# Optimization experiments

Hardware: AMD Instinct MI355X
Metric: run time of the kernel (lower is better)

## Reference

```python
import jax, jax.numpy as jnp
import numpy as np

T = 2048          # tokens (flattened prefill)
H = 3584          # hidden_size
NH = 16           # num query heads
NKV = 8           # num kv heads
G = NH // NKV     # GQA group size
D = 256           # head_dim
SCALE = 256.0 ** -0.5   # query_pre_attn_scalar ** -0.5
WINDOW = 1024     # sliding_window_size
CAP = 50.0        # logit softcap
BASE = 10000.0    # rope theta
NEG = -1e30


def _rope(x, positions):
    # x: [T, n, D], neox-style rotary over full head_dim
    half = D // 2
    inv_freq = 1.0 / (BASE ** (jnp.arange(0, D, 2, dtype=jnp.float32) / D))  # [half]
    ang = positions.astype(jnp.float32)[:, None] * inv_freq  # [T, half]
    cos = jnp.cos(ang)[:, None, :]  # [T,1,half]
    sin = jnp.sin(ang)[:, None, :]
    x1, x2 = x[..., :half], x[..., half:]
    return jnp.concatenate([x1 * cos - x2 * sin, x2 * cos + x1 * sin], axis=-1)


def setup_inputs() -> dict:
    key = jax.random.key(0)
    ks = jax.random.split(key, 5)
    s = 0.02
    return {
        "hidden_states": jax.random.normal(ks[0], (T, H), dtype=jnp.float32),
        "Wq": jax.random.normal(ks[1], (H, NH * D), dtype=jnp.float32) * s,
        "Wk": jax.random.normal(ks[2], (H, NKV * D), dtype=jnp.float32) * s,
        "Wv": jax.random.normal(ks[3], (H, NKV * D), dtype=jnp.float32) * s,
        "Wo": jax.random.normal(ks[4], (NH * D, H), dtype=jnp.float32) * s,
        "positions": jnp.arange(T, dtype=jnp.int32),
    }


def reference(hidden_states, Wq, Wk, Wv, Wo, positions):
    q = (hidden_states @ Wq).reshape(T, NH, D)
    k = (hidden_states @ Wk).reshape(T, NKV, D)
    v = (hidden_states @ Wv).reshape(T, NKV, D)
    q = _rope(q, positions)
    k = _rope(k, positions)

    # GQA attention: group query heads over kv heads
    qg = (q * SCALE).reshape(T, NKV, G, D)
    scores = jnp.einsum('qhgd,khd->hgqk', qg, k)  # [NKV,G,T,T]
    scores = CAP * jnp.tanh(scores / CAP)         # logit softcap

    i = jnp.arange(T)[:, None]
    j = jnp.arange(T)[None, :]
    mask = (j <= i) & (i - j < WINDOW)            # causal + sliding window
    scores = jnp.where(mask, scores, NEG)

    p = jax.nn.softmax(scores, axis=-1)
    o = jnp.einsum('hgqk,khd->qhgd', p, v).reshape(T, NH * D)
    return o @ Wo
```

## Files before the change

### kernel.cpp

```cpp
#include <hip/hip_runtime.h>
#include <math.h>

typedef __attribute__((ext_vector_type(8))) __bf16 bf16x8;
typedef __attribute__((ext_vector_type(4))) __bf16 bf16x4;
typedef __attribute__((ext_vector_type(4))) float f32x4;

#define TSEQ 2048
#define HDIM 3584
#define NQH  16
#define NKVH 8
#define DH   256
#define WIN  1024
#define QKD  (NQH * DH)
#define KVD  (NKVH * DH)
#define QLD  8256
#define OLD  4160
#define WOLD 4160
#define VLD  2112

#define MFMA __builtin_amdgcn_mfma_f32_16x16x32_bf16

__device__ __forceinline__ void gload_lds16(const void* g, void* l) {
  __builtin_amdgcn_global_load_lds(
      (const __attribute__((address_space(1))) void*)g,
      (__attribute__((address_space(3))) void*)l, 16, 0, 0);
}


__global__ void cvt_bf16_kernel(const float* __restrict__ in,
                                __bf16* __restrict__ out, long n) {
  long i = ((long)blockIdx.x * blockDim.x + threadIdx.x) * 4;
  if (i >= n) return;
  float4 v = *reinterpret_cast<const float4*>(in + i);
  bf16x4 o4;
  o4.x = (__bf16)v.x; o4.y = (__bf16)v.y; o4.z = (__bf16)v.z; o4.w = (__bf16)v.w;
  *reinterpret_cast<bf16x4*>(out + i) = o4;
}

__global__ void transpose_all_kernel(const float* __restrict__ Wq,
                                     const float* __restrict__ Wk,
                                     const float* __restrict__ Wv,
                                     const float* __restrict__ Wo,
                                     __bf16* __restrict__ WqT,
                                     __bf16* __restrict__ WkT,
                                     __bf16* __restrict__ WvT,
                                     __bf16* __restrict__ WoT) {
  __shared__ float tile[64][65];
  int id = blockIdx.x;
  const float* src; __bf16* dst; int R, C, ldo;
  if (id < 3584)      { src = Wq; dst = WqT; R = HDIM; C = QKD; ldo = HDIM; }
  else if (id < 5376) { id -= 3584; src = Wk; dst = WkT; R = HDIM; C = KVD; ldo = HDIM; }
  else if (id < 7168) { id -= 5376; src = Wv; dst = WvT; R = HDIM; C = KVD; ldo = HDIM; }
  else                { id -= 7168; src = Wo; dst = WoT; R = QKD; C = HDIM; ldo = WOLD; }
  const int nbx = C >> 6;
  const int c0 = (id % nbx) * 64, r0 = (id / nbx) * 64;
  const int tid = threadIdx.x;
#pragma unroll
  for (int it = 0; it < 4; ++it) {
    int f = tid + it * 256;
    int row = f >> 4, c4 = (f & 15) * 4;
    float4 v = *reinterpret_cast<const float4*>(&src[(size_t)(r0 + row) * C + c0 + c4]);
    tile[row][c4] = v.x; tile[row][c4 + 1] = v.y;
    tile[row][c4 + 2] = v.z; tile[row][c4 + 3] = v.w;
  }
  __syncthreads();
#pragma unroll
  for (int it = 0; it < 2; ++it) {
    int s = tid + it * 256;
    int oc = s >> 3, rb = (s & 7) * 8;
    bf16x8 o8;
#pragma unroll
    for (int j = 0; j < 8; ++j) o8[j] = (__bf16)tile[rb + j][oc];
    *reinterpret_cast<bf16x8*>(&dst[(size_t)(c0 + oc) * ldo + r0 + rb]) = o8;
  }
}

__global__ void transpose_bf16_kernel(const __bf16* __restrict__ in,
                                      __bf16* __restrict__ out, int ldin, int ldout) {
  __shared__ __bf16 tile[32][33];
  const int tx = threadIdx.x, ty = threadIdx.y;
  const int c0 = blockIdx.x * 32, r0 = blockIdx.y * 32;
#pragma unroll
  for (int i = 0; i < 4; ++i)
    tile[ty + i * 8][tx] = in[(size_t)(r0 + ty + i * 8) * ldin + (c0 + tx)];
  __syncthreads();
#pragma unroll
  for (int i = 0; i < 4; ++i)
    out[(size_t)(c0 + ty + i * 8) * ldout + (r0 + tx)] = tile[tx][ty + i * 8];
}

__global__ void rope_table_kernel(const int* __restrict__ positions,
                                  float* __restrict__ ct,
                                  float* __restrict__ st) {
  int i = blockIdx.x * blockDim.x + threadIdx.x;
  if (i >= TSEQ * 128) return;
  int t = i >> 7, j = i & 127;
  float invf = (float)exp((double)(-2 * j) * (9.210340371976184 / 256.0));
  float ang = (float)positions[t] * invf;
  ct[i] = cosf(ang);
  st[i] = sinf(ang);
}

__global__ void rope_qk_kernel(__bf16* __restrict__ qkv,
                               const float* __restrict__ ct,
                               const float* __restrict__ st) {
  int i = blockIdx.x * blockDim.x + threadIdx.x;
  int jg = (i & 15) * 8;
  int th = i >> 4;
  int t = th / 24;
  int hh = th - t * 24;
  float scale = (hh < 16) ? 0.0625f : 1.0f;
  size_t base = (size_t)t * QLD + ((hh < 16) ? hh * DH : QKD + (hh - 16) * DH) + jg;
  bf16x8 x1 = *reinterpret_cast<const bf16x8*>(qkv + base);
  bf16x8 x2 = *reinterpret_cast<const bf16x8*>(qkv + base + 128);
  const float* cp = ct + (t << 7) + jg;
  const float* sp = st + (t << 7) + jg;
  bf16x8 o1, o2;
#pragma unroll
  for (int e = 0; e < 8; ++e) {
    float c = cp[e], s = sp[e];
    float a = (float)x1[e], b = (float)x2[e];
    o1[e] = (__bf16)((a * c - b * s) * scale);
    o2[e] = (__bf16)((b * c + a * s) * scale);
  }
  *reinterpret_cast<bf16x8*>(qkv + base) = o1;
  *reinterpret_cast<bf16x8*>(qkv + base + 128) = o2;
}

__global__ void reduce2_kernel(const __bf16* __restrict__ p0,
                               const __bf16* __restrict__ p1,
                               float* __restrict__ out, int n8) {
  int stride = gridDim.x * blockDim.x;
  for (int i = blockIdx.x * blockDim.x + threadIdx.x; i < n8; i += stride) {
    bf16x8 a = reinterpret_cast<const bf16x8*>(p0)[i];
    bf16x8 b = reinterpret_cast<const bf16x8*>(p1)[i];
    float4 o0, o1;
    o0.x = (float)a[0] + (float)b[0]; o0.y = (float)a[1] + (float)b[1];
    o0.z = (float)a[2] + (float)b[2]; o0.w = (float)a[3] + (float)b[3];
    o1.x = (float)a[4] + (float)b[4]; o1.y = (float)a[5] + (float)b[5];
    o1.z = (float)a[6] + (float)b[6]; o1.w = (float)a[7] + (float)b[7];
    reinterpret_cast<float4*>(out)[2 * i] = o0;
    reinterpret_cast<float4*>(out)[2 * i + 1] = o1;
  }
}


__device__ __forceinline__ void stage_half(const __bf16* __restrict__ gbase,
                                           int row0, int ldg, int k0,
                                           __bf16* lds_half, int tid) {
  const int lane = tid & 63;
  const int w = tid >> 6;
  const int lr = lane >> 3;
  const int swzcol = ((lane & 7) ^ lr) << 3;
  const __bf16* g = gbase + (size_t)(row0 + w * 8 + lr) * ldg + k0 + swzcol;
  __bf16* l = lds_half + w * 512;
  gload_lds16(g, l);
  gload_lds16(g + (size_t)64 * ldg, l + 4096);
}

#define BAR __builtin_amdgcn_s_barrier()

#define RD_A(DST, BASE, MO)                                         \
  _Pragma("unroll")                                                 \
  for (int m_ = 0; m_ < 4; ++m_) {                                  \
    const __bf16* p_ = (BASE) + (((MO) + m_) * 16 + l15) * 64;      \
    DST[m_][0] = *(const bf16x8*)(p_ + kxa);                        \
    DST[m_][1] = *(const bf16x8*)(p_ + kxb);                        \
  }

#define RD_B(DST, BASE, NO)                                         \
  _Pragma("unroll")                                                 \
  for (int n_ = 0; n_ < 2; ++n_) {                                  \
    const __bf16* p_ = (BASE) + (bro + ((NO) + n_) * 16 + l15) * 64;\
    DST[n_][0] = *(const bf16x8*)(p_ + kxa);                        \
    DST[n_][1] = *(const bf16x8*)(p_ + kxb);                        \
  }

#define MQUAD(AF, BF, MO, NO)                                          \
  __builtin_amdgcn_s_setprio(1);                                       \
  _Pragma("unroll")                                                    \
  for (int m_ = 0; m_ < 4; ++m_)                                       \
    _Pragma("unroll")                                                  \
    for (int n_ = 0; n_ < 2; ++n_) {                                   \
      acc[(MO) + m_][(NO) + n_] =                                      \
          MFMA(AF[m_][0], BF[n_][0], acc[(MO) + m_][(NO) + n_], 0, 0, 0); \
      acc[(MO) + m_][(NO) + n_] =                                      \
          MFMA(AF[m_][1], BF[n_][1], acc[(MO) + m_][(NO) + n_], 0, 0, 0); \
    }                                                                  \
  __builtin_amdgcn_s_setprio(0);

template <typename CT>
__global__ __launch_bounds__(512, 2) void gemm256_kernel(
    const __bf16* __restrict__ A, const __bf16* __restrict__ B,
    CT* __restrict__ C, int lda, int Klen, int ldc, int nrc, size_t cstride) {
  __shared__ __bf16 lds[2][2][2][8192];

  const int nwg = gridDim.x;
  const int per = nwg >> 3;
  const int wg = (blockIdx.x & 7) * per + (blockIdx.x >> 3);
  const int kslice = wg / nrc;
  const int rem = wg - kslice * nrc;
  const int row0 = (rem & 7) * 256;
  const int col0 = (rem >> 3) * 256;
  const int k0 = kslice * Klen;
  CT* Cs = C + (size_t)kslice * cstride;

  const int tid = threadIdx.x;
  const int lane = tid & 63, w = tid >> 6;
  const int wr = w >> 2, wc = w & 3;
  const int l15 = lane & 15, lg = lane >> 4;
  const int swz = (lane & 7) << 3;
  const int kxa = (lg * 8) ^ swz;
  const int kxb = (32 + lg * 8) ^ swz;
  const int bro = (wc & 1) * 64;

  const __bf16* Ablk = A + (size_t)row0 * lda + k0;
  const __bf16* Bblk = B + (size_t)col0 * lda + k0;

  const __bf16* Ae = &lds[0][0][wr][0];
  const __bf16* Be = &lds[0][1][wc >> 1][0];
  const __bf16* Ao = &lds[1][0][wr][0];
  const __bf16* Bo = &lds[1][1][wc >> 1][0];

  f32x4 acc[8][4] = {};
  const int NT = Klen >> 6;
  const int NI = NT >> 1;

  stage_half(Ablk, 0,   lda, 0,  &lds[0][0][0][0], tid);
  stage_half(Ablk, 128, lda, 0,  &lds[0][0][1][0], tid);
  stage_half(Bblk, 0,   lda, 0,  &lds[0][1][0][0], tid);
  stage_half(Bblk, 128, lda, 0,  &lds[0][1][1][0], tid);
  stage_half(Ablk, 0,   lda, 64, &lds[1][0][0][0], tid);
  stage_half(Ablk, 128, lda, 64, &lds[1][0][1][0], tid);
  asm volatile("s_waitcnt vmcnt(4)" ::: "memory");
  BAR;

  bf16x8 a03[4][2], a47[4][2], b01[2][2], b23[2][2];

  for (int j = 0; j < NI; ++j) {
    const int e = 2 * j, o = 2 * j + 1;
    const bool last = (j == NI - 1);

    RD_A(a03, Ae, 0);
    RD_B(b01, Be, 0);
    stage_half(Bblk, 0, lda, o * 64, &lds[1][1][0][0], tid);
    asm volatile("s_waitcnt lgkmcnt(8)" ::: "memory");
    BAR; MQUAD(a03, b01, 0, 0); BAR;

    RD_A(a47, Ae, 4);
    stage_half(Bblk, 128, lda, o * 64, &lds[1][1][1][0], tid);
    BAR; MQUAD(a47, b01, 4, 0); BAR;

    RD_B(b23, Be, 2);
    if (!last) stage_half(Ablk, 0, lda, (e + 2) * 64, &lds[0][0][0][0], tid);
    BAR; MQUAD(a47, b23, 4, 2); BAR;

    if (!last) {
      stage_half(Ablk, 128, lda, (e + 2) * 64, &lds[0][0][1][0], tid);
      asm volatile("s_waitcnt vmcnt(4)" ::: "memory");
    } else {
      asm volatile("s_waitcnt vmcnt(0)" ::: "memory");
    }
    BAR; MQUAD(a03, b23, 0, 2); BAR;

    RD_A(a03, Ao, 0);
    RD_B(b01, Bo, 0);
    if (!last) stage_half(Bblk, 0, lda, (e + 2) * 64, &lds[0][1][0][0], tid);
    asm volatile("s_waitcnt lgkmcnt(8)" ::: "memory");
    BAR; MQUAD(a03, b01, 0, 0); BAR;

    RD_A(a47, Ao, 4);
    if (!last) stage_half(Bblk, 128, lda, (e + 2) * 64, &lds[0][1][1][0], tid);
    BAR; MQUAD(a47, b01, 4, 0); BAR;

    RD_B(b23, Bo, 2);
    if (!last) stage_half(Ablk, 0, lda, (o + 2) * 64, &lds[1][0][0][0], tid);
    BAR; MQUAD(a47, b23, 4, 2); BAR;

    if (!last) {
      stage_half(Ablk, 128, lda, (o + 2) * 64, &lds[1][0][1][0], tid);
      asm volatile("s_waitcnt vmcnt(4)" ::: "memory");
    }
    BAR; MQUAD(a03, b23, 0, 2); BAR;
  }

#pragma unroll
  for (int m = 0; m < 8; ++m)
#pragma unroll
    for (int n = 0; n < 4; ++n)
#pragma unroll
      for (int r = 0; r < 4; ++r) {
        int row = row0 + wr * 128 + m * 16 + lg * 4 + r;
        int col = col0 + wc * 64 + n * 16 + l15;
        Cs[(size_t)row * ldc + col] = (CT)acc[m][n][r];
      }
}


__device__ __forceinline__ void attn_stage(const __bf16* __restrict__ kg,
                                           const __bf16* __restrict__ vg,
                                           __bf16* Kd, __bf16* Vd, int tid) {
#pragma unroll
  for (int i = 0; i < 8; ++i) {
    int c = tid + i * 256;
    int krow = c >> 5, kslot = c & 31;
    gload_lds16(kg + (size_t)krow * QLD + ((kslot ^ (krow & 7)) * 8), Kd + c * 8);
    int vrow = c >> 3, vslot = c & 7;
    gload_lds16(vg + (size_t)vrow * VLD + ((vslot ^ (vrow & 7)) * 8), Vd + c * 8);
  }
}

__global__ __launch_bounds__(256, 2) void attn_kernel(
    const __bf16* __restrict__ q, const __bf16* __restrict__ k,
    const __bf16* __restrict__ vt, __bf16* __restrict__ o) {
  __shared__ __bf16 Klds[64][256];
  __shared__ __bf16 Vlds[256][64];
  __shared__ __bf16 Plds[4][16][72];

  const int tid = threadIdx.x;
  const int wave = tid >> 6;
  const int lane = tid & 63;
  const int l16 = lane & 15;
  const int lg = lane >> 4;
  const int h = blockIdx.x;
  const int qh = 2 * h + (blockIdx.y & 1);
  const int q0 = (31 - (int)(blockIdx.y >> 1)) << 6;
  const int qr = q0 + wave * 16;

  const __bf16* kg0 = k + (size_t)h * DH;
  const __bf16* vg0 = vt + (size_t)(h * DH) * VLD;

  int t_lo = q0 - (WIN - 1);
  if (t_lo < 0) t_lo = 0;
  t_lo &= ~63;
  const int NTile = ((q0 - t_lo) >> 6) + 1;

  bf16x8 qf[8];
  {
    const __bf16* qp = q + (size_t)(qr + l16) * QLD + qh * DH + lg * 8;
#pragma unroll
    for (int ds = 0; ds < 8; ++ds)
      qf[ds] = *reinterpret_cast<const bf16x8*>(qp + ds * 32);
  }

  f32x4 accO[16] = {};
  float l_run[4] = {0.f, 0.f, 0.f, 0.f};

  for (int it = 0; it < NTile; ++it) {
    const int t0 = t_lo + it * 64;

    attn_stage(kg0 + (size_t)t0 * QLD, vg0 + t0, &Klds[0][0], &Vlds[0][0], tid);
    asm volatile("s_waitcnt vmcnt(0)" ::: "memory");
    __builtin_amdgcn_s_barrier();

    f32x4 accS[4] = {};
    __builtin_amdgcn_s_setprio(1);
#pragma unroll
    for (int ds = 0; ds < 8; ++ds)
#pragma unroll
      for (int nt = 0; nt < 4; ++nt) {
        int row = nt * 16 + l16;
        int slot = (4 * ds + lg) ^ (l16 & 7);
        bf16x8 kf = *reinterpret_cast<const bf16x8*>(&Klds[0][0] + row * 256 + slot * 8);
        accS[nt] = MFMA(qf[ds], kf, accS[nt], 0, 0, 0);
      }
    __builtin_amdgcn_s_setprio(0);

    float rs[4] = {0.f, 0.f, 0.f, 0.f};
#pragma unroll
    for (int nt = 0; nt < 4; ++nt) {
      int key = t0 + nt * 16 + l16;
#pragma unroll
      for (int r = 0; r < 4; ++r) {
        int row = qr + lg * 4 + r;
        float t = __expf(accS[nt][r] * 0.04f);
        float p = __expf(-100.0f / (t + 1.0f));
        bool valid = (key <= row) && (row - key < WIN);
        p = valid ? p : 0.f;
        rs[r] += p;
        Plds[wave][lg * 4 + r][nt * 16 + l16] = (__bf16)p;
      }
    }
#pragma unroll
    for (int off = 1; off < 16; off <<= 1)
#pragma unroll
      for (int r = 0; r < 4; ++r)
        rs[r] += __shfl_xor(rs[r], off);
#pragma unroll
    for (int r = 0; r < 4; ++r)
      l_run[r] += rs[r];

    __builtin_amdgcn_s_setprio(1);
#pragma unroll
    for (int ks = 0; ks < 2; ++ks) {
      bf16x8 pa = *reinterpret_cast<const bf16x8*>(&Plds[wave][l16][ks * 32 + lg * 8]);
#pragma unroll
      for (int nt2 = 0; nt2 < 16; ++nt2) {
        int row = nt2 * 16 + l16;
        int slot = (4 * ks + lg) ^ (l16 & 7);
        bf16x8 vb = *reinterpret_cast<const bf16x8*>(&Vlds[0][0] + row * 64 + slot * 8);
        accO[nt2] = MFMA(pa, vb, accO[nt2], 0, 0, 0);
      }
    }
    __builtin_amdgcn_s_setprio(0);
    __builtin_amdgcn_s_barrier();
  }

#pragma unroll
  for (int r = 0; r < 4; ++r) {
    float inv_l = 1.f / l_run[r];
    int row = qr + lg * 4 + r;
#pragma unroll
    for (int nt2 = 0; nt2 < 16; ++nt2)
      o[(size_t)row * OLD + qh * DH + nt2 * 16 + l16] = (__bf16)(accO[nt2][r] * inv_l);
  }
}


extern "C" void kernel_launch(void* const* d_in, const int* in_sizes, int n_in,
                              void* d_out, int out_size, void* d_ws, size_t ws_size,
                              hipStream_t stream) {
  const float* hs = (const float*)d_in[0];
  const float* Wq = (const float*)d_in[1];
  const float* Wk = (const float*)d_in[2];
  const float* Wv = (const float*)d_in[3];
  const float* Wo = (const float*)d_in[4];
  const int* positions = (const int*)d_in[5];
  float* out = (float*)d_out;

  char* ws = (char*)d_ws;
  const size_t SZ_HS  = (size_t)TSEQ * HDIM * 2;
  const size_t SZ_WQT = (size_t)QKD * HDIM * 2;
  const size_t SZ_WKT = (size_t)KVD * HDIM * 2;
  const size_t SZ_WOT = (size_t)HDIM * WOLD * 2;
  const size_t SZ_QKV = (size_t)TSEQ * QLD * 2;
  const size_t SZ_O   = (size_t)TSEQ * OLD * 2;
  const size_t SZ_TBL = (size_t)TSEQ * 128 * 4;

  __bf16* hs_bf = (__bf16*)ws; ws += SZ_HS;
  __bf16* WqT   = (__bf16*)ws; ws += SZ_WQT;
  __bf16* WkT   = (__bf16*)ws; ws += SZ_WKT;
  __bf16* WvT   = (__bf16*)ws; ws += SZ_WKT;
  __bf16* WoT   = (__bf16*)ws; ws += SZ_WOT;
  __bf16* qkv   = (__bf16*)ws; ws += SZ_QKV;
  __bf16* o_bf  = (__bf16*)ws; ws += SZ_O;
  float*  cost  = (float*)ws;  ws += SZ_TBL;
  float*  sint  = (float*)ws;  ws += SZ_TBL;
  __bf16* vt_bf = hs_bf;
  __bf16* cpart = WqT;
  if ((size_t)(ws - (char*)d_ws) > ws_size) return;

  cvt_bf16_kernel<<<(TSEQ * HDIM) / 1024, 256, 0, stream>>>(hs, hs_bf, (long)TSEQ * HDIM);
  transpose_all_kernel<<<10752, 256, 0, stream>>>(Wq, Wk, Wv, Wo, WqT, WkT, WvT, WoT);
  rope_table_kernel<<<(TSEQ * 128) / 256, 256, 0, stream>>>(positions, cost, sint);

  gemm256_kernel<__bf16><<<256, 512, 0, stream>>>(hs_bf, WqT, qkv, HDIM, HDIM, QLD, 256, 0);

  rope_qk_kernel<<<(TSEQ * 24 * 16) / 256, 256, 0, stream>>>(qkv, cost, sint);
  transpose_bf16_kernel<<<dim3(KVD / 32, TSEQ / 32), dim3(32, 8), 0, stream>>>(qkv + QKD + KVD, vt_bf, QLD, VLD);

  attn_kernel<<<dim3(NKVH, 64), 256, 0, stream>>>(qkv, qkv + QKD, vt_bf, o_bf);

  gemm256_kernel<__bf16><<<224, 512, 0, stream>>>(o_bf, WoT, cpart, OLD, QKD / 2, HDIM, 112,
                                                  (size_t)TSEQ * HDIM);
  reduce2_kernel<<<2048, 256, 0, stream>>>(cpart, cpart + (size_t)TSEQ * HDIM, out,
                                           TSEQ * HDIM / 8);
}
```

Before: 304.4 us.

## Replace split-K output projection with 128x256-tile GEMM writing fp32 directly

The output projection previously ran as a split-K GEMM with 256x256 tiles into two bf16 partial buffers, followed by a separate reduction kernel. It now uses a new 128x256-tile GEMM over the full K that writes fp32 output directly, which removes the partial-buffer traffic, the reduce launch and one bf16 rounding. The new kernel uses a different LDS double-buffer pipeline and allows one workgroup per CU. Each workgroup now runs twice as many K iterations on a smaller tile, which lowers MFMA work per LDS load.

```diff
diff --git a/kernel.cpp b/kernel.cpp
--- a/kernel.cpp
+++ b/kernel.cpp
@@ -127,23 +127,6 @@
   *reinterpret_cast<bf16x8*>(qkv + base + 128) = o2;
 }
 
-__global__ void reduce2_kernel(const __bf16* __restrict__ p0,
-                               const __bf16* __restrict__ p1,
-                               float* __restrict__ out, int n8) {
-  int stride = gridDim.x * blockDim.x;
-  for (int i = blockIdx.x * blockDim.x + threadIdx.x; i < n8; i += stride) {
-    bf16x8 a = reinterpret_cast<const bf16x8*>(p0)[i];
-    bf16x8 b = reinterpret_cast<const bf16x8*>(p1)[i];
-    float4 o0, o1;
-    o0.x = (float)a[0] + (float)b[0]; o0.y = (float)a[1] + (float)b[1];
-    o0.z = (float)a[2] + (float)b[2]; o0.w = (float)a[3] + (float)b[3];
-    o1.x = (float)a[4] + (float)b[4]; o1.y = (float)a[5] + (float)b[5];
-    o1.z = (float)a[6] + (float)b[6]; o1.w = (float)a[7] + (float)b[7];
-    reinterpret_cast<float4*>(out)[2 * i] = o0;
-    reinterpret_cast<float4*>(out)[2 * i + 1] = o1;
-  }
-}
-
 
 __device__ __forceinline__ void stage_half(const __bf16* __restrict__ gbase,
                                            int row0, int ldg, int k0,
@@ -189,33 +172,29 @@
     }                                                                  \
   __builtin_amdgcn_s_setprio(0);
 
-template <typename CT>
 __global__ __launch_bounds__(512, 2) void gemm256_kernel(
     const __bf16* __restrict__ A, const __bf16* __restrict__ B,
-    CT* __restrict__ C, int lda, int Klen, int ldc, int nrc, size_t cstride) {
+    __bf16* __restrict__ C, int lda, int Klen, int ldc, int nrc) {
   __shared__ __bf16 lds[2][2][2][8192];
 
   const int nwg = gridDim.x;
   const int per = nwg >> 3;
   const int wg = (blockIdx.x & 7) * per + (blockIdx.x >> 3);
-  const int kslice = wg / nrc;
-  const int rem = wg - kslice * nrc;
+  const int rem = wg % nrc;
   const int row0 = (rem & 7) * 256;
   const int col0 = (rem >> 3) * 256;
-  const int k0 = kslice * Klen;
-  CT* Cs = C + (size_t)kslice * cstride;
+  __bf16* Cs = C;
 
   const int tid = threadIdx.x;
   const int lane = tid & 63, w = tid >> 6;
   const int wr = w >> 2, wc = w & 3;
   const int l15 = lane & 15, lg = lane >> 4;
-  const int swz = (lane & 7) << 3;
-  const int kxa = (lg * 8) ^ swz;
-  const int kxb = (32 + lg * 8) ^ swz;
+  const int kxa = (lg * 8) ^ ((lane & 7) << 3);
+  const int kxb = (32 + lg * 8) ^ ((lane & 7) << 3);
   const int bro = (wc & 1) * 64;
 
-  const __bf16* Ablk = A + (size_t)row0 * lda + k0;
-  const __bf16* Bblk = B + (size_t)col0 * lda + k0;
+  const __bf16* Ablk = A + (size_t)row0 * lda;
+  const __bf16* Bblk = B + (size_t)col0 * lda;
 
   const __bf16* Ae = &lds[0][0][wr][0];
   const __bf16* Be = &lds[0][1][wc >> 1][0];
@@ -292,7 +271,99 @@
       for (int r = 0; r < 4; ++r) {
         int row = row0 + wr * 128 + m * 16 + lg * 4 + r;
         int col = col0 + wc * 64 + n * 16 + l15;
-        Cs[(size_t)row * ldc + col] = (CT)acc[m][n][r];
+        Cs[(size_t)row * ldc + col] = (__bf16)acc[m][n][r];
+      }
+}
+
+__global__ __launch_bounds__(512, 1) void gemm128_kernel(
+    const __bf16* __restrict__ A, const __bf16* __restrict__ B,
+    float* __restrict__ C, int lda, int Klen, int ldc) {
+  __shared__ __bf16 lds[2][3][8192];
+
+  const int per = gridDim.x >> 3;
+  const int wg = (blockIdx.x & 7) * per + (blockIdx.x >> 3);
+  const int row0 = (wg & 15) * 128;
+  const int col0 = (wg >> 4) * 256;
+
+  const int tid = threadIdx.x;
+  const int lane = tid & 63, w = tid >> 6;
+  const int wr = w >> 2, wc = w & 3;
+  const int l15 = lane & 15, lg = lane >> 4;
+  const int kxa = (lg * 8) ^ ((lane & 7) << 3);
+  const int kxb = (32 + lg * 8) ^ ((lane & 7) << 3);
+  const int bro = (wc & 1) * 64;
+
+  const __bf16* Ablk = A + (size_t)row0 * lda;
+  const __bf16* Bblk = B + (size_t)col0 * lda;
+
+  f32x4 acc[4][4] = {};
+  const int NT = Klen >> 6;
+
+  stage_half(Ablk, 0,   lda, 0,  &lds[0][0][0], tid);
+  stage_half(Bblk, 0,   lda, 0,  &lds[0][1][0], tid);
+  stage_half(Bblk, 128, lda, 0,  &lds[0][2][0], tid);
+  stage_half(Ablk, 0,   lda, 64, &lds[1][0][0], tid);
+  asm volatile("s_waitcnt vmcnt(2)" ::: "memory");
+  BAR;
+
+  bf16x8 a03[4][2], b01[2][2], b23[2][2];
+
+  for (int t = 0; t < NT; ++t) {
+    const int cur = t & 1, nxt = cur ^ 1;
+    const __bf16* Ah = &lds[cur][0][0];
+    const __bf16* Bh = &lds[cur][1 + (wc >> 1)][0];
+
+    {
+      const int MO = wr * 4;
+#pragma unroll
+      for (int m_ = 0; m_ < 4; ++m_) {
+        const __bf16* p_ = Ah + ((MO + m_) * 16 + l15) * 64;
+        a03[m_][0] = *(const bf16x8*)(p_ + kxa);
+        a03[m_][1] = *(const bf16x8*)(p_ + kxb);
+      }
+    }
+    RD_B(b01, Bh, 0);
+    RD_B(b23, Bh, 2);
+
+    if (t + 1 < NT) {
+      stage_half(Bblk, 0,   lda, (t + 1) * 64, &lds[nxt][1][0], tid);
+      stage_half(Bblk, 128, lda, (t + 1) * 64, &lds[nxt][2][0], tid);
+    }
+
+    asm volatile("s_waitcnt lgkmcnt(0)" ::: "memory");
+    BAR;
+    if (t + 2 < NT) stage_half(Ablk, 0, lda, (t + 2) * 64, &lds[cur][0][0], tid);
+
+    __builtin_amdgcn_s_setprio(1);
+#pragma unroll
+    for (int m_ = 0; m_ < 4; ++m_) {
+#pragma unroll
+      for (int n_ = 0; n_ < 2; ++n_) {
+        acc[m_][n_] = MFMA(a03[m_][0], b01[n_][0], acc[m_][n_], 0, 0, 0);
+        acc[m_][n_] = MFMA(a03[m_][1], b01[n_][1], acc[m_][n_], 0, 0, 0);
+        acc[m_][n_ + 2] = MFMA(a03[m_][0], b23[n_][0], acc[m_][n_ + 2], 0, 0, 0);
+        acc[m_][n_ + 2] = MFMA(a03[m_][1], b23[n_][1], acc[m_][n_ + 2], 0, 0, 0);
+      }
+    }
+    __builtin_amdgcn_s_setprio(0);
+
+    if (t + 2 < NT) {
+      asm volatile("s_waitcnt vmcnt(2)" ::: "memory");
+    } else {
+      asm volatile("s_waitcnt vmcnt(0)" ::: "memory");
+    }
+    BAR;
+  }
+
+#pragma unroll
+  for (int m = 0; m < 4; ++m)
+#pragma unroll
+    for (int n = 0; n < 4; ++n)
+#pragma unroll
+      for (int r = 0; r < 4; ++r) {
+        int row = row0 + wr * 64 + m * 16 + lg * 4 + r;
+        int col = col0 + wc * 64 + n * 16 + l15;
+        C[(size_t)row * ldc + col] = acc[m][n][r];
       }
 }
 
@@ -447,22 +518,18 @@
   float*  cost  = (float*)ws;  ws += SZ_TBL;
   float*  sint  = (float*)ws;  ws += SZ_TBL;
   __bf16* vt_bf = hs_bf;
-  __bf16* cpart = WqT;
   if ((size_t)(ws - (char*)d_ws) > ws_size) return;
 
   cvt_bf16_kernel<<<(TSEQ * HDIM) / 1024, 256, 0, stream>>>(hs, hs_bf, (long)TSEQ * HDIM);
   transpose_all_kernel<<<10752, 256, 0, stream>>>(Wq, Wk, Wv, Wo, WqT, WkT, WvT, WoT);
   rope_table_kernel<<<(TSEQ * 128) / 256, 256, 0, stream>>>(positions, cost, sint);
 
-  gemm256_kernel<__bf16><<<256, 512, 0, stream>>>(hs_bf, WqT, qkv, HDIM, HDIM, QLD, 256, 0);
+  gemm256_kernel<<<256, 512, 0, stream>>>(hs_bf, WqT, qkv, HDIM, HDIM, QLD, 256);
 
   rope_qk_kernel<<<(TSEQ * 24 * 16) / 256, 256, 0, stream>>>(qkv, cost, sint);
   transpose_bf16_kernel<<<dim3(KVD / 32, TSEQ / 32), dim3(32, 8), 0, stream>>>(qkv + QKD + KVD, vt_bf, QLD, VLD);
 
   attn_kernel<<<dim3(NKVH, 64), 256, 0, stream>>>(qkv, qkv + QKD, vt_bf, o_bf);
 
-  gemm256_kernel<__bf16><<<224, 512, 0, stream>>>(o_bf, WoT, cpart, OLD, QKD / 2, HDIM, 112,
-                                                  (size_t)TSEQ * HDIM);
-  reduce2_kernel<<<2048, 256, 0, stream>>>(cpart, cpart + (size_t)TSEQ * HDIM, out,
-                                           TSEQ * HDIM / 8);
-}
+  gemm128_kernel<<<224, 512, 0, stream>>>(o_bf, WoT, out, OLD, QKD, HDIM);
+}
```

New measurement: 305.8 us. Within noise of the previous version (+0.5%).
